# Performance work log

Hardware: AMD Instinct MI355X
Metric: run time of the kernel (lower is better)

Reference implementation:

```python
import jax, jax.numpy as jnp
import numpy as np

B, DIM, H, W = 32, 512, 48, 24


def conv1x1(x, w, b):
    # x: [B,C,H,W], w: [O,C], b: [O]  (torch Conv2d 1x1 weight squeezed)
    return jnp.einsum('bchw,oc->bohw', x, w) + b[None, :, None, None]


def setup_inputs() -> dict:
    key = jax.random.key(0)
    ks = jax.random.split(key, 14)
    s = 0.02
    inp = {
        'x': jax.random.normal(ks[0], (B, DIM, H, W), jnp.float32),
        'x_h': jax.random.normal(ks[1], (B, DIM, H, W), jnp.float32),
        'Wg': jax.random.normal(ks[2], (DIM, DIM), jnp.float32) * s,
        'bg': jax.random.normal(ks[3], (DIM,), jnp.float32) * s,
        'Wt': jax.random.normal(ks[4], (DIM, DIM), jnp.float32) * s,
        'bt': jax.random.normal(ks[5], (DIM,), jnp.float32) * s,
        'Wp': jax.random.normal(ks[6], (DIM, DIM), jnp.float32) * s,
        'bp': jax.random.normal(ks[7], (DIM,), jnp.float32) * s,
        'Ww': jax.random.normal(ks[8], (DIM, DIM), jnp.float32) * s,
        'bw': jax.random.normal(ks[9], (DIM,), jnp.float32) * s,
        'gamma': jax.random.normal(ks[10], (DIM,), jnp.float32) * 0.1,
        'beta': jax.random.normal(ks[11], (DIM,), jnp.float32) * 0.1,
        'run_mean': jax.random.normal(ks[12], (DIM,), jnp.float32) * 0.1,
        'run_var': jax.random.uniform(ks[13], (DIM,), jnp.float32, 0.5, 1.5),
    }
    return inp


def reference(x, x_h, Wg, bg, Wt, bt, Wp, bp, Ww, bw, gamma, beta, run_mean, run_var):
    Bsz, dim = x.shape[0], Wg.shape[0]
    g_x = conv1x1(x_h, Wg, bg).reshape(Bsz, dim, -1)      # [B,dim,N]
    theta_x = conv1x1(x, Wt, bt).reshape(Bsz, dim, -1)    # [B,dim,N]
    phi_x = conv1x1(x_h, Wp, bp).reshape(Bsz, dim, -1)    # [B,dim,N]
    # energy[b,i,j] = sum_n theta[b,i,n] * phi[b,j,n]  -> channel attention [B,dim,dim]
    energy = jnp.einsum('bin,bjn->bij', theta_x, phi_x)
    attention = energy / dim  # energy.size(-1) == dim
    y = jnp.einsum('bij,bjn->bin', attention, g_x).reshape(Bsz, dim, *x_h.shape[2:])
    W_y = conv1x1(y, Ww, bw)
    # BatchNorm2d in eval mode
    inv = gamma / jnp.sqrt(run_var + 1e-5)
    W_y = (W_y - run_mean[None, :, None, None]) * inv[None, :, None, None] + beta[None, :, None, None]
    return W_y + x
```

## Files before the change

kernel.cpp:

```cpp
#include <hip/hip_runtime.h>
#include <stdint.h>

typedef short short8 __attribute__((ext_vector_type(8)));
typedef float f32x4 __attribute__((ext_vector_type(4)));
typedef unsigned short u16;
typedef unsigned int u32;

struct alignas(8) U16x4 { u16 x, y, z, w; };

__device__ __forceinline__ u16 f2bf(float f) {
  u32 u = __float_as_uint(f);
  u += 0x7fffu + ((u >> 16) & 1u);
  return (u16)(u >> 16);
}
__device__ __forceinline__ float bf2f(u16 v) {
  return __uint_as_float(((u32)v) << 16);
}

__device__ __forceinline__ void gld_lds16(const u16* g, u16* l) {
  __builtin_amdgcn_global_load_lds((const __attribute__((address_space(1))) u32*)g,
                                   (__attribute__((address_space(3))) u32*)l,
                                   16, 0, 0);
}

__device__ __forceinline__ void mfma16x16x32(f32x4& c, short8 a, short8 b) {
  asm("v_mfma_f32_16x16x32_bf16 %0, %1, %2, %0" : "+v"(c) : "v"(a), "v"(b));
}

__device__ __forceinline__ float wave_red(float v) {
  for (int off = 32; off; off >>= 1) v += __shfl_down(v, off);
  return v;
}

template<int EPI>
__global__ void __launch_bounds__(512, 2) gemm_abt(
                         const u16* __restrict__ A, int64_t Abs,
                         const u16* __restrict__ Bt, int64_t Bbs,
                         void* __restrict__ Cptr, int64_t Cbs,
                         int M, int N, int K,
                         const float* __restrict__ v1,
                         const float* __restrict__ v2,
                         const float* __restrict__ v3,
                         const float* __restrict__ v4,
                         const u16* __restrict__ xres) {
  constexpr int BM = 256, BN = 128, BK = 32;
  __shared__ u16 As[2][BM * BK];
  __shared__ u16 Bs[2][BN * BK];

  int bx, by, b;
  if (gridDim.z == 1) {
    const int nbx = N >> 7;
    const int bpb = nbx * (M >> 8);
    const int id = blockIdx.x;
    const int xcd = id & 7, rest = id >> 3;
    b = xcd + 8 * (rest / bpb);
    const int wi = rest % bpb;
    by = wi / nbx; bx = wi % nbx;
  } else {
    bx = blockIdx.x; by = blockIdx.y; b = blockIdx.z;
  }

  const u16* Ab = A + (int64_t)b * Abs;
  const u16* Bb = Bt + (int64_t)b * Bbs;
  const int brow = by * BM, bcol = bx * BN;
  const int tid = threadIdx.x, lane = tid & 63, w = tid >> 6;
  const int wr = w >> 1, wc = w & 1;

  f32x4 acc[4][4] = {};

  const int sr = tid >> 2;
  const int scs = ((tid & 3) ^ (sr & 3)) * 8;
  u16* lA0 = &As[0][sr * BK + (tid & 3) * 8];
  u16* lB0 = &Bs[0][sr * BK + (tid & 3) * 8];
  const u16* gA = Ab + (int64_t)(brow + sr) * K + scs;
  const u16* gB = Bb + (int64_t)(bcol + sr) * K + scs;

  const int la16 = lane & 15;
  const int kg = (lane >> 4) * 8;
  const int kc = kg ^ ((la16 & 3) * 8);
  const int nt = K / BK;

  gld_lds16(gA, lA0);
  gld_lds16(gA + (int64_t)128 * K, lA0 + 128 * BK);
  gld_lds16(gB, lB0);

  for (int t = 0; t < nt; ++t) {
    __builtin_amdgcn_s_barrier();
    if (t + 1 < nt) {
      const int nb = (t + 1) & 1;
      const int k0 = (t + 1) * BK;
      u16* la = lA0 + nb * BM * BK;
      u16* lb = lB0 + nb * BN * BK;
      gld_lds16(gA + k0, la);
      gld_lds16(gA + (int64_t)128 * K + k0, la + 128 * BK);
      gld_lds16(gB + k0, lb);
      asm volatile("s_waitcnt vmcnt(3)" ::: "memory");
    } else {
      asm volatile("s_waitcnt vmcnt(0)" ::: "memory");
    }
    __builtin_amdgcn_s_barrier();
    __builtin_amdgcn_sched_barrier(0);
    const u16* as = As[t & 1];
    const u16* bs = Bs[t & 1];
    short8 af[4], bf[4];
#pragma unroll
    for (int m = 0; m < 4; ++m)
      af[m] = *(const short8*)&as[(wr * 64 + m * 16 + la16) * BK + kc];
#pragma unroll
    for (int n = 0; n < 4; ++n)
      bf[n] = *(const short8*)&bs[(wc * 64 + n * 16 + la16) * BK + kc];
#pragma unroll
    for (int m = 0; m < 4; ++m)
#pragma unroll
      for (int n = 0; n < 4; ++n)
        mfma16x16x32(acc[m][n], af[m], bf[n]);
  }
  asm volatile("s_nop 7\n\ts_nop 7");

  const int r0 = brow + wr * 64 + (lane >> 4) * 4;
  const int c0 = bcol + wc * 64 + la16;
  const int64_t b512 = (int64_t)b * 512;

  if (EPI == 4) {
    float* Cb = (float*)Cptr + (int64_t)b * Cbs;
    const u16* xb = xres + (int64_t)b * Cbs;
#pragma unroll
    for (int m = 0; m < 4; ++m) {
#pragma unroll
      for (int r = 0; r < 4; ++r) {
        const int row = r0 + m * 16 + r;
        const float scl = v1[row], shf = v2[b512 + row];
#pragma unroll
        for (int n = 0; n < 4; ++n) {
          const int col = c0 + n * 16;
          Cb[(int64_t)row * N + col] =
              acc[m][n][r] * scl + shf + bf2f(xb[(int64_t)row * N + col]);
        }
      }
    }
  } else {
    u16* Cb = (u16*)Cptr + (int64_t)b * Cbs;
#pragma unroll
    for (int m = 0; m < 4; ++m) {
#pragma unroll
      for (int r = 0; r < 4; ++r) {
        const int row = r0 + m * 16 + r;
        float a1 = 0.f, a3 = 0.f;
        if (EPI == 6) { a1 = v1[b512 + row]; a3 = v3[row]; }
#pragma unroll
        for (int n = 0; n < 4; ++n) {
          const int col = c0 + n * 16;
          float v = acc[m][n][r];
          if (EPI == 6) v += a1 * v2[col] + a3 * v4[b512 + col];
          Cb[(int64_t)row * N + col] = f2bf(v);
        }
      }
    }
  }
}

__global__ void cvt_row(const float* __restrict__ in, u16* __restrict__ out,
                        float* __restrict__ rowsum) {
  const int64_t row = blockIdx.x;
  const float4* ib = (const float4*)(in + row * 1152);
  U16x4* ob = (U16x4*)(out + row * 1152);
  float s = 0.f;
  for (int i = threadIdx.x; i < 288; i += 256) {
    float4 v = ib[i];
    s += v.x + v.y + v.z + v.w;
    U16x4 o = {f2bf(v.x), f2bf(v.y), f2bf(v.z), f2bf(v.w)};
    ob[i] = o;
  }
  s = wave_red(s);
  __shared__ float red[4];
  if ((threadIdx.x & 63) == 0) red[threadIdx.x >> 6] = s;
  __syncthreads();
  if (threadIdx.x == 0) rowsum[row] = red[0] + red[1] + red[2] + red[3];
}

__global__ void prep_xh(const float* __restrict__ xh, u16* __restrict__ xhB,
                        u16* __restrict__ xhT, float* __restrict__ rxh_part) {
  __shared__ float tl[32][33];
  const int b = blockIdx.z;
  const int n0 = blockIdx.x * 32, c0 = blockIdx.y * 32;
  const float* ib = xh + (int64_t)b * 589824;
  const int tr = threadIdx.x >> 3, tc = (threadIdx.x & 7) * 4;
  const float4 v = *(const float4*)&ib[(int64_t)(c0 + tr) * 1152 + n0 + tc];
  tl[tr][tc] = v.x; tl[tr][tc + 1] = v.y; tl[tr][tc + 2] = v.z; tl[tr][tc + 3] = v.w;
  U16x4 o = {f2bf(v.x), f2bf(v.y), f2bf(v.z), f2bf(v.w)};
  *(U16x4*)&xhB[(int64_t)b * 589824 + (int64_t)(c0 + tr) * 1152 + n0 + tc] = o;
  __syncthreads();
  U16x4 ot = {f2bf(tl[tc][tr]), f2bf(tl[tc + 1][tr]),
              f2bf(tl[tc + 2][tr]), f2bf(tl[tc + 3][tr])};
  *(U16x4*)&xhT[(int64_t)b * 589824 + (int64_t)(n0 + tr) * 512 + c0 + tc] = ot;
  if (threadIdx.x < 32) {
    float s = 0;
#pragma unroll
    for (int c = 0; c < 32; ++c) s += tl[threadIdx.x][c];
    rxh_part[(n0 >> 5) * 16384 + b * 512 + c0 + threadIdx.x] = s;
  }
}

__global__ void transpose_cvt4(const float* __restrict__ s0, const float* __restrict__ s1,
                               const float* __restrict__ s2, const float* __restrict__ s3,
                               u16* __restrict__ d0, u16* __restrict__ d1,
                               u16* __restrict__ d2, u16* __restrict__ d3) {
  const int z = blockIdx.z;
  const float* in = z == 0 ? s0 : z == 1 ? s1 : z == 2 ? s2 : s3;
  u16* out = z == 0 ? d0 : z == 1 ? d1 : z == 2 ? d2 : d3;
  __shared__ float t[32][33];
  const int n0 = blockIdx.x * 32, c0 = blockIdx.y * 32;
  const int tr = threadIdx.x >> 3, tc = (threadIdx.x & 7) * 4;
  const float4 v = *(const float4*)&in[(int64_t)(c0 + tr) * 512 + n0 + tc];
  t[tr][tc] = v.x; t[tr][tc + 1] = v.y; t[tr][tc + 2] = v.z; t[tr][tc + 3] = v.w;
  __syncthreads();
  U16x4 o;
  o.x = f2bf(t[tc][tr]); o.y = f2bf(t[tc + 1][tr]);
  o.z = f2bf(t[tc + 2][tr]); o.w = f2bf(t[tc + 3][tr]);
  *(U16x4*)&out[(int64_t)(n0 + tr) * 512 + c0 + tc] = o;
}

__global__ void cvt_kernel(const float* __restrict__ in, u16* __restrict__ out, int n4) {
  const int i = blockIdx.x * 256 + threadIdx.x;
  if (i < n4) {
    const float4 v = ((const float4*)in)[i];
    U16x4 o = {f2bf(v.x), f2bf(v.y), f2bf(v.z), f2bf(v.w)};
    ((U16x4*)out)[i] = o;
  }
}

__global__ void k_misc(const float* __restrict__ rxh_part, float* __restrict__ rxh,
                       const float* __restrict__ gamma, const float* __restrict__ beta,
                       const float* __restrict__ mean, const float* __restrict__ var,
                       const float* __restrict__ bw,
                       const float* __restrict__ bp, const float* __restrict__ bg,
                       float* __restrict__ sc2, float* __restrict__ shift0,
                       float* __restrict__ s2) {
  if (blockIdx.x < 64) {
    const int i = blockIdx.x * 256 + threadIdx.x;
    float s = 0;
#pragma unroll 4
    for (int p = 0; p < 36; ++p) s += rxh_part[p * 16384 + i];
    rxh[i] = s;
  } else {
    for (int c = threadIdx.x; c < 512; c += 256) {
      const float sc = gamma[c] * rsqrtf(var[c] + 1e-5f);
      sc2[c] = sc * (1.0f / 512.0f);
      shift0[c] = (bw[c] - mean[c]) * sc + beta[c];
    }
    if (threadIdx.x < 64) {
      float p = 0;
      for (int k = threadIdx.x; k < 512; k += 64) p += bp[k] * bg[k];
      p = wave_red(p);
      if (threadIdx.x == 0) s2[0] = p;
    }
  }
}

__global__ void k_mv1(const float* __restrict__ Wp, const float* __restrict__ Wt,
                      const float* __restrict__ Ww,
                      const u16* __restrict__ WpT, const u16* __restrict__ WgT,
                      const float* __restrict__ bg, const float* __restrict__ bt,
                      const float* __restrict__ bp,
                      const float* __restrict__ rx, const float* __restrict__ rxh,
                      float* __restrict__ sigphi, float* __restrict__ tau2,
                      float* __restrict__ h1, float* __restrict__ w1,
                      float* __restrict__ c2) {
  const int wid = blockIdx.x * 4 + (threadIdx.x >> 6);
  const int lane = threadIdx.x & 63;
  float dot = 0;
  if (wid < 16384) {
    const int b = wid >> 9, t = wid & 511;
    const float* wr = Wp + (int64_t)t * 512;
    const float* vr = rxh + b * 512;
#pragma unroll
    for (int k = 0; k < 8; ++k) dot += wr[lane + k * 64] * vr[lane + k * 64];
    dot = wave_red(dot);
    if (lane == 0) sigphi[wid] = dot;
  } else if (wid < 32768) {
    const int r = wid - 16384, b = r >> 9, t = r & 511;
    const float* wr = Wt + (int64_t)t * 512;
    const float* vr = rx + b * 512;
#pragma unroll
    for (int k = 0; k < 8; ++k) dot += wr[lane + k * 64] * vr[lane + k * 64];
    dot = wave_red(dot);
    if (lane == 0) tau2[r] = dot + 1152.0f * bt[t];
  } else if (wid < 33280) {
    const int j = wid - 32768;
    const u16* wr = WpT + (int64_t)j * 512;
#pragma unroll
    for (int k = 0; k < 8; ++k) dot += bf2f(wr[lane + k * 64]) * bg[lane + k * 64];
    dot = wave_red(dot);
    if (lane == 0) h1[j] = dot;
  } else if (wid < 33792) {
    const int c = wid - 33280;
    const float* wr = Ww + (int64_t)c * 512;
#pragma unroll
    for (int k = 0; k < 8; ++k) dot += wr[lane + k * 64] * bt[lane + k * 64];
    dot = wave_red(dot);
    if (lane == 0) w1[c] = dot;
  } else {
    const int e = wid - 33792;
    const u16* wr = WgT + (int64_t)e * 512;
#pragma unroll
    for (int k = 0; k < 8; ++k) dot += bf2f(wr[lane + k * 64]) * bp[lane + k * 64];
    dot = wave_red(dot);
    if (lane == 0) c2[e] = dot;
  }
}

__global__ void k_mv2(const u16* __restrict__ WgT, const float* __restrict__ Ww,
                      const float* __restrict__ bg,
                      const float* __restrict__ sigphi, const float* __restrict__ tau2,
                      float* __restrict__ c1, float* __restrict__ w2,
                      float* __restrict__ s1) {
  const int wid = blockIdx.x * 4 + (threadIdx.x >> 6);
  const int lane = threadIdx.x & 63;
  float dot = 0;
  if (wid < 16384) {
    const int b = wid >> 9, t = wid & 511;
    const u16* wr = WgT + (int64_t)t * 512;
    const float* vr = sigphi + b * 512;
#pragma unroll
    for (int k = 0; k < 8; ++k) dot += bf2f(wr[lane + k * 64]) * vr[lane + k * 64];
    dot = wave_red(dot);
    if (lane == 0) c1[wid] = dot;
  } else if (wid < 32768) {
    const int r = wid - 16384, b = r >> 9, t = r & 511;
    const float* wr = Ww + (int64_t)t * 512;
    const float* vr = tau2 + b * 512;
#pragma unroll
    for (int k = 0; k < 8; ++k) dot += wr[lane + k * 64] * vr[lane + k * 64];
    dot = wave_red(dot);
    if (lane == 0) w2[r] = dot;
  } else if (wid < 32800) {
    const int b = wid - 32768;
    const float* vr = sigphi + b * 512;
#pragma unroll
    for (int k = 0; k < 8; ++k) dot += vr[lane + k * 64] * bg[lane + k * 64];
    dot = wave_red(dot);
    if (lane == 0) s1[b] = dot;
  }
}

__global__ void k_shiftv(const u16* __restrict__ R, const float* __restrict__ h1,
                         const float* __restrict__ w1, const float* __restrict__ w2,
                         const float* __restrict__ s1, const float* __restrict__ s2,
                         const float* __restrict__ sc2, const float* __restrict__ shift0,
                         float* __restrict__ shiftv) {
  const int wid = blockIdx.x * 4 + (threadIdx.x >> 6);
  const int lane = threadIdx.x & 63;
  const int b = wid >> 9, c = wid & 511;
  const u16* rr = R + (int64_t)b * 262144 + (int64_t)c * 512;
  float dot = 0;
#pragma unroll
  for (int k = 0; k < 8; ++k) dot += bf2f(rr[lane + k * 64]) * h1[lane + k * 64];
  dot = wave_red(dot);
  if (lane == 0)
    shiftv[wid] = sc2[c] * (dot + s1[b] * w1[c] + s2[0] * w2[wid]) + shift0[c];
}

extern "C" void kernel_launch(void* const* d_in, const int* in_sizes, int n_in,
                              void* d_out, int out_size, void* d_ws, size_t ws_size,
                              hipStream_t stream) {
  const float* x     = (const float*)d_in[0];
  const float* x_h   = (const float*)d_in[1];
  const float* Wg    = (const float*)d_in[2];
  const float* bg    = (const float*)d_in[3];
  const float* Wt    = (const float*)d_in[4];
  const float* bt    = (const float*)d_in[5];
  const float* Wp    = (const float*)d_in[6];
  const float* bp    = (const float*)d_in[7];
  const float* Ww    = (const float*)d_in[8];
  const float* bw    = (const float*)d_in[9];
  const float* gamma = (const float*)d_in[10];
  const float* beta  = (const float*)d_in[11];
  const float* rmean = (const float*)d_in[12];
  const float* rvar  = (const float*)d_in[13];
  float* out = (float*)d_out;

  const int Bsz = 32, D = 512, N = 1152;
  const int64_t DN = (int64_t)D * N;
  const int64_t DD = (int64_t)D * D;

  char* ws = (char*)d_ws;
  const size_t KB = 1024, MB = 1048576;
  u16* WtT  = (u16*)(ws + 0);
  u16* WpT  = (u16*)(ws + 512 * KB);
  u16* WwB  = (u16*)(ws + 1 * MB);
  u16* WgT  = (u16*)(ws + 1 * MB + 512 * KB);
  u16* WaB  = (u16*)(ws + 2 * MB);
  u16* WbTB = (u16*)(ws + 2 * MB + 512 * KB);
  u16* WwT  = (u16*)(ws + 3 * MB);
  float* rx     = (float*)(ws + 3 * MB + 512 * KB);
  float* rxh    = (float*)(ws + 3 * MB + 576 * KB);
  float* sigphi = (float*)(ws + 3 * MB + 640 * KB);
  float* tau2   = (float*)(ws + 3 * MB + 704 * KB);
  float* c1     = (float*)(ws + 3 * MB + 768 * KB);
  float* w2     = (float*)(ws + 3 * MB + 832 * KB);
  float* shiftv = (float*)(ws + 3 * MB + 896 * KB);
  float* h1     = (float*)(ws + 3 * MB + 960 * KB);
  float* w1     = (float*)(ws + 3 * MB + 962 * KB);
  float* c2     = (float*)(ws + 3 * MB + 964 * KB);
  float* sc2    = (float*)(ws + 3 * MB + 968 * KB);
  float* shift0 = (float*)(ws + 3 * MB + 970 * KB);
  float* s1     = (float*)(ws + 3 * MB + 972 * KB);
  float* s2     = (float*)(ws + 3 * MB + 974 * KB);
  u16* xB  = (u16*)(ws + 4 * MB);
  u16* xhB = (u16*)(ws + 40 * MB);
  u16* xhT = (u16*)(ws + 76 * MB);
  u16* SD1 = (u16*)(ws + 112 * MB);
  u16* SD2 = (u16*)(ws + 130 * MB);
  float* rxh_part = (float*)(ws + 148 * MB);

  cvt_row<<<dim3(Bsz * D), 256, 0, stream>>>(x, xB, rx);
  prep_xh<<<dim3(36, 16, Bsz), 256, 0, stream>>>(x_h, xhB, xhT, rxh_part);
  transpose_cvt4<<<dim3(16, 16, 4), 256, 0, stream>>>(Wt, Wp, Wg, Ww, WtT, WpT, WgT, WwT);
  cvt_kernel<<<dim3(D * D / 4 / 256), 256, 0, stream>>>(Ww, WwB, D * D / 4);
  k_misc<<<dim3(65), 256, 0, stream>>>(rxh_part, rxh, gamma, beta, rmean, rvar, bw,
                                       bp, bg, sc2, shift0, s2);
  k_mv1<<<dim3(8576), 256, 0, stream>>>(Wp, Wt, Ww, WpT, WgT, bg, bt, bp, rx, rxh,
                                        sigphi, tau2, h1, w1, c2);
  k_mv2<<<dim3(8200), 256, 0, stream>>>(WgT, Ww, bg, sigphi, tau2, c1, w2, s1);
  gemm_abt<0><<<dim3(4, 2, 2), 512, 0, stream>>>(
      WwB, DD, WtT, DD, WaB, DD, D, D, D, nullptr, nullptr, nullptr, nullptr, nullptr);

  gemm_abt<0><<<dim3(8 * Bsz), 512, 0, stream>>>(
      xhB, DN, xB, DN, SD1, DD, D, D, N, nullptr, nullptr, nullptr, nullptr, nullptr);
  gemm_abt<0><<<dim3(8 * Bsz), 512, 0, stream>>>(
      WaB, 0, SD1, DD, SD2, DD, D, D, D, nullptr, nullptr, nullptr, nullptr, nullptr);
  k_shiftv<<<dim3(4096), 256, 0, stream>>>(SD2, h1, w1, w2, s1, s2, sc2, shift0, shiftv);
  gemm_abt<6><<<dim3(8 * Bsz), 512, 0, stream>>>(
      SD2, DD, WbTB, 0, SD1, DD, D, D, D, w2, c2, w1, c1, nullptr);
  gemm_abt<4><<<dim3(18 * Bsz), 512, 0, stream>>>(
      SD1, DD, xhT, DN, out, DN, D, N, D, sc2, shiftv, nullptr, nullptr, xB);
}
```

Before: 225.2 us.

## Deepen GEMM LDS pipeline to four stages and fuse input prep kernels

The GEMM moves from a double-buffered to a four-buffer LDS ring filled by global_load_lds. Up to three tiles are in flight, with matching vmcnt waits, and s_setprio raises wave priority around the MFMA block. The separate x row-convert and x_h transpose-convert kernels are merged into one prep_all kernel with 64x64 tiles that also writes partial row sums for both inputs, which k_misc then reduces. The ring needs 96KB of dynamic LDS per block, which likely drops the two-blocks-per-CU occupancy implied by the launch bounds, trading occupancy for latency hiding.

```diff
diff --git a/kernel.cpp b/kernel.cpp
--- a/kernel.cpp
+++ b/kernel.cpp
@@ -44,8 +44,9 @@
                          const float* __restrict__ v4,
                          const u16* __restrict__ xres) {
   constexpr int BM = 256, BN = 128, BK = 32;
-  __shared__ u16 As[2][BM * BK];
-  __shared__ u16 Bs[2][BN * BK];
+  extern __shared__ u16 lds[];
+  u16* ldsA = lds;
+  u16* ldsB = lds + 4 * (BM * BK);
 
   int bx, by, b;
   if (gridDim.z == 1) {
@@ -70,8 +71,7 @@
 
   const int sr = tid >> 2;
   const int scs = ((tid & 3) ^ (sr & 3)) * 8;
-  u16* lA0 = &As[0][sr * BK + (tid & 3) * 8];
-  u16* lB0 = &Bs[0][sr * BK + (tid & 3) * 8];
+  const int lo = sr * BK + (tid & 3) * 8;
   const u16* gA = Ab + (int64_t)(brow + sr) * K + scs;
   const u16* gB = Bb + (int64_t)(bcol + sr) * K + scs;
 
@@ -80,28 +80,34 @@
   const int kc = kg ^ ((la16 & 3) * 8);
   const int nt = K / BK;
 
-  gld_lds16(gA, lA0);
-  gld_lds16(gA + (int64_t)128 * K, lA0 + 128 * BK);
-  gld_lds16(gB, lB0);
+#define STAGE(buf, k0)                                              \
+  do {                                                              \
+    u16* la_ = ldsA + (buf) * (BM * BK) + lo;                       \
+    u16* lb_ = ldsB + (buf) * (BN * BK) + lo;                       \
+    gld_lds16(gA + (k0), la_);                                      \
+    gld_lds16(gA + (int64_t)128 * K + (k0), la_ + 128 * BK);        \
+    gld_lds16(gB + (k0), lb_);                                      \
+  } while (0)
+
+  STAGE(0, 0);
+  STAGE(1, BK);
+  STAGE(2, 2 * BK);
 
   for (int t = 0; t < nt; ++t) {
     __builtin_amdgcn_s_barrier();
-    if (t + 1 < nt) {
-      const int nb = (t + 1) & 1;
-      const int k0 = (t + 1) * BK;
-      u16* la = lA0 + nb * BM * BK;
-      u16* lb = lB0 + nb * BN * BK;
-      gld_lds16(gA + k0, la);
-      gld_lds16(gA + (int64_t)128 * K + k0, la + 128 * BK);
-      gld_lds16(gB + k0, lb);
-      asm volatile("s_waitcnt vmcnt(3)" ::: "memory");
+    if (t + 3 < nt) {
+      STAGE((t + 3) & 3, (t + 3) * BK);
+      asm volatile("s_waitcnt vmcnt(9)" ::: "memory");
     } else {
-      asm volatile("s_waitcnt vmcnt(0)" ::: "memory");
+      const int rem = nt - 1 - t;
+      if (rem == 2)      asm volatile("s_waitcnt vmcnt(6)" ::: "memory");
+      else if (rem == 1) asm volatile("s_waitcnt vmcnt(3)" ::: "memory");
+      else               asm volatile("s_waitcnt vmcnt(0)" ::: "memory");
     }
     __builtin_amdgcn_s_barrier();
     __builtin_amdgcn_sched_barrier(0);
-    const u16* as = As[t & 1];
-    const u16* bs = Bs[t & 1];
+    const u16* as = ldsA + (t & 3) * (BM * BK);
+    const u16* bs = ldsB + (t & 3) * (BN * BK);
     short8 af[4], bf[4];
 #pragma unroll
     for (int m = 0; m < 4; ++m)
@@ -109,12 +115,15 @@
 #pragma unroll
     for (int n = 0; n < 4; ++n)
       bf[n] = *(const short8*)&bs[(wc * 64 + n * 16 + la16) * BK + kc];
+    __builtin_amdgcn_s_setprio(1);
 #pragma unroll
     for (int m = 0; m < 4; ++m)
 #pragma unroll
       for (int n = 0; n < 4; ++n)
         mfma16x16x32(acc[m][n], af[m], bf[n]);
-  }
+    __builtin_amdgcn_s_setprio(0);
+  }
+#undef STAGE
   asm volatile("s_nop 7\n\ts_nop 7");
 
   const int r0 = brow + wr * 64 + (lane >> 4) * 4;
@@ -159,45 +168,48 @@
   }
 }
 
-__global__ void cvt_row(const float* __restrict__ in, u16* __restrict__ out,
-                        float* __restrict__ rowsum) {
-  const int64_t row = blockIdx.x;
-  const float4* ib = (const float4*)(in + row * 1152);
-  U16x4* ob = (U16x4*)(out + row * 1152);
-  float s = 0.f;
-  for (int i = threadIdx.x; i < 288; i += 256) {
-    float4 v = ib[i];
-    s += v.x + v.y + v.z + v.w;
+__global__ void prep_all(const float* __restrict__ x, const float* __restrict__ xh,
+                         u16* __restrict__ xB, u16* __restrict__ xhB,
+                         u16* __restrict__ xhT,
+                         float* __restrict__ rx_part, float* __restrict__ rxh_part) {
+  __shared__ float tl[64][65];
+  __shared__ float rs[64];
+  const int z = blockIdx.z;
+  const int b = z & 31;
+  const bool isxh = z >= 32;
+  const float* src = (isxh ? xh : x) + (int64_t)b * 589824;
+  u16* dstB = (isxh ? xhB : xB) + (int64_t)b * 589824;
+  const int n0 = blockIdx.x * 64, c0 = blockIdx.y * 64;
+  const int t = threadIdx.x;
+  const int cl = t >> 4;
+  const int q = t & 15;
+#pragma unroll
+  for (int p = 0; p < 4; ++p) {
+    const int row = p * 16 + cl;
+    const float4 v = *(const float4*)&src[(int64_t)(c0 + row) * 1152 + n0 + q * 4];
+    tl[row][q * 4] = v.x; tl[row][q * 4 + 1] = v.y;
+    tl[row][q * 4 + 2] = v.z; tl[row][q * 4 + 3] = v.w;
     U16x4 o = {f2bf(v.x), f2bf(v.y), f2bf(v.z), f2bf(v.w)};
-    ob[i] = o;
-  }
-  s = wave_red(s);
-  __shared__ float red[4];
-  if ((threadIdx.x & 63) == 0) red[threadIdx.x >> 6] = s;
+    *(U16x4*)&dstB[(int64_t)(c0 + row) * 1152 + n0 + q * 4] = o;
+    float pr = v.x + v.y + v.z + v.w;
+    pr += __shfl_down(pr, 8); pr += __shfl_down(pr, 4);
+    pr += __shfl_down(pr, 2); pr += __shfl_down(pr, 1);
+    if (q == 0) rs[row] = pr;
+  }
   __syncthreads();
-  if (threadIdx.x == 0) rowsum[row] = red[0] + red[1] + red[2] + red[3];
-}
-
-__global__ void prep_xh(const float* __restrict__ xh, u16* __restrict__ xhB,
-                        u16* __restrict__ xhT, float* __restrict__ rxh_part) {
-  __shared__ float tl[32][33];
-  const int b = blockIdx.z;
-  const int n0 = blockIdx.x * 32, c0 = blockIdx.y * 32;
-  const float* ib = xh + (int64_t)b * 589824;
-  const int tr = threadIdx.x >> 3, tc = (threadIdx.x & 7) * 4;
-  const float4 v = *(const float4*)&ib[(int64_t)(c0 + tr) * 1152 + n0 + tc];
-  tl[tr][tc] = v.x; tl[tr][tc + 1] = v.y; tl[tr][tc + 2] = v.z; tl[tr][tc + 3] = v.w;
-  U16x4 o = {f2bf(v.x), f2bf(v.y), f2bf(v.z), f2bf(v.w)};
-  *(U16x4*)&xhB[(int64_t)b * 589824 + (int64_t)(c0 + tr) * 1152 + n0 + tc] = o;
-  __syncthreads();
-  U16x4 ot = {f2bf(tl[tc][tr]), f2bf(tl[tc + 1][tr]),
-              f2bf(tl[tc + 2][tr]), f2bf(tl[tc + 3][tr])};
-  *(U16x4*)&xhT[(int64_t)b * 589824 + (int64_t)(n0 + tr) * 512 + c0 + tc] = ot;
-  if (threadIdx.x < 32) {
-    float s = 0;
-#pragma unroll
-    for (int c = 0; c < 32; ++c) s += tl[threadIdx.x][c];
-    rxh_part[(n0 >> 5) * 16384 + b * 512 + c0 + threadIdx.x] = s;
+  if (t < 64) {
+    float* part = isxh ? rxh_part : rx_part;
+    part[blockIdx.x * 16384 + b * 512 + c0 + t] = rs[t];
+  }
+  if (isxh) {
+    const int n = t >> 2, cb = (t & 3) * 16;
+    u16* dT = xhT + (int64_t)b * 589824 + (int64_t)(n0 + n) * 512 + c0 + cb;
+#pragma unroll
+    for (int j = 0; j < 4; ++j) {
+      U16x4 o = {f2bf(tl[cb + 4 * j][n]), f2bf(tl[cb + 4 * j + 1][n]),
+                 f2bf(tl[cb + 4 * j + 2][n]), f2bf(tl[cb + 4 * j + 3][n])};
+      *(U16x4*)&dT[4 * j] = o;
+    }
   }
 }
 
@@ -229,7 +241,8 @@
   }
 }
 
-__global__ void k_misc(const float* __restrict__ rxh_part, float* __restrict__ rxh,
+__global__ void k_misc(const float* __restrict__ rx_part, const float* __restrict__ rxh_part,
+                       float* __restrict__ rx, float* __restrict__ rxh,
                        const float* __restrict__ gamma, const float* __restrict__ beta,
                        const float* __restrict__ mean, const float* __restrict__ var,
                        const float* __restrict__ bw,
@@ -239,9 +252,15 @@
   if (blockIdx.x < 64) {
     const int i = blockIdx.x * 256 + threadIdx.x;
     float s = 0;
-#pragma unroll 4
-    for (int p = 0; p < 36; ++p) s += rxh_part[p * 16384 + i];
+#pragma unroll 3
+    for (int p = 0; p < 18; ++p) s += rxh_part[p * 16384 + i];
     rxh[i] = s;
+  } else if (blockIdx.x < 128) {
+    const int i = (blockIdx.x - 64) * 256 + threadIdx.x;
+    float s = 0;
+#pragma unroll 3
+    for (int p = 0; p < 18; ++p) s += rx_part[p * 16384 + i];
+    rx[i] = s;
   } else {
     for (int c = threadIdx.x; c < 512; c += 256) {
       const float sc = gamma[c] * rsqrtf(var[c] + 1e-5f);
@@ -382,6 +401,7 @@
   const int Bsz = 32, D = 512, N = 1152;
   const int64_t DN = (int64_t)D * N;
   const int64_t DD = (int64_t)D * D;
+  const size_t LDSB = 98304;
 
   char* ws = (char*)d_ws;
   const size_t KB = 1024, MB = 1048576;
@@ -391,7 +411,6 @@
   u16* WgT  = (u16*)(ws + 1 * MB + 512 * KB);
   u16* WaB  = (u16*)(ws + 2 * MB);
   u16* WbTB = (u16*)(ws + 2 * MB + 512 * KB);
-  u16* WwT  = (u16*)(ws + 3 * MB);
   float* rx     = (float*)(ws + 3 * MB + 512 * KB);
   float* rxh    = (float*)(ws + 3 * MB + 576 * KB);
   float* sigphi = (float*)(ws + 3 * MB + 640 * KB);
@@ -411,27 +430,29 @@
   u16* xhT = (u16*)(ws + 76 * MB);
   u16* SD1 = (u16*)(ws + 112 * MB);
   u16* SD2 = (u16*)(ws + 130 * MB);
-  float* rxh_part = (float*)(ws + 148 * MB);
-
-  cvt_row<<<dim3(Bsz * D), 256, 0, stream>>>(x, xB, rx);
-  prep_xh<<<dim3(36, 16, Bsz), 256, 0, stream>>>(x_h, xhB, xhT, rxh_part);
-  transpose_cvt4<<<dim3(16, 16, 4), 256, 0, stream>>>(Wt, Wp, Wg, Ww, WtT, WpT, WgT, WwT);
+  float* rx_part  = (float*)(ws + 148 * MB);
+  float* rxh_part = (float*)(ws + 150 * MB);
+
+  prep_all<<<dim3(18, 8, 64), 256, 0, stream>>>(x, x_h, xB, xhB, xhT,
+                                                rx_part, rxh_part);
+  transpose_cvt4<<<dim3(16, 16, 4), 256, 0, stream>>>(Wt, Wp, Wg, Ww, WtT, WpT, WgT,
+                                                      (u16*)(ws + 152 * MB) );
   cvt_kernel<<<dim3(D * D / 4 / 256), 256, 0, stream>>>(Ww, WwB, D * D / 4);
-  k_misc<<<dim3(65), 256, 0, stream>>>(rxh_part, rxh, gamma, beta, rmean, rvar, bw,
-                                       bp, bg, sc2, shift0, s2);
+  k_misc<<<dim3(129), 256, 0, stream>>>(rx_part, rxh_part, rx, rxh, gamma, beta,
+                                        rmean, rvar, bw, bp, bg, sc2, shift0, s2);
   k_mv1<<<dim3(8576), 256, 0, stream>>>(Wp, Wt, Ww, WpT, WgT, bg, bt, bp, rx, rxh,
                                         sigphi, tau2, h1, w1, c2);
   k_mv2<<<dim3(8200), 256, 0, stream>>>(WgT, Ww, bg, sigphi, tau2, c1, w2, s1);
-  gemm_abt<0><<<dim3(4, 2, 2), 512, 0, stream>>>(
+  gemm_abt<0><<<dim3(4, 2, 2), 512, LDSB, stream>>>(
       WwB, DD, WtT, DD, WaB, DD, D, D, D, nullptr, nullptr, nullptr, nullptr, nullptr);
 
-  gemm_abt<0><<<dim3(8 * Bsz), 512, 0, stream>>>(
+  gemm_abt<0><<<dim3(8 * Bsz), 512, LDSB, stream>>>(
       xhB, DN, xB, DN, SD1, DD, D, D, N, nullptr, nullptr, nullptr, nullptr, nullptr);
-  gemm_abt<0><<<dim3(8 * Bsz), 512, 0, stream>>>(
+  gemm_abt<0><<<dim3(8 * Bsz), 512, LDSB, stream>>>(
       WaB, 0, SD1, DD, SD2, DD, D, D, D, nullptr, nullptr, nullptr, nullptr, nullptr);
   k_shiftv<<<dim3(4096), 256, 0, stream>>>(SD2, h1, w1, w2, s1, s2, sc2, shift0, shiftv);
-  gemm_abt<6><<<dim3(8 * Bsz), 512, 0, stream>>>(
+  gemm_abt<6><<<dim3(8 * Bsz), 512, LDSB, stream>>>(
       SD2, DD, WbTB, 0, SD1, DD, D, D, D, w2, c2, w1, c1, nullptr);
-  gemm_abt<4><<<dim3(18 * Bsz), 512, 0, stream>>>(
+  gemm_abt<4><<<dim3(18 * Bsz), 512, LDSB, stream>>>(
       SD1, DD, xhT, DN, out, DN, D, N, D, sc2, shiftv, nullptr, nullptr, xB);
 }
```

Result: faster. 208.2 us (-7.5%).
